# Kernel tuning notes

Hardware: AMD Instinct MI355X
Metric: run time of the kernel (lower is better)

The kernel has to match this reference:

```python
import jax, jax.numpy as jnp
import numpy as np

KERNEL_MUL = 2.0
KERNEL_NUM = 5
FIX_SIGMA = None


def setup_inputs() -> dict:
    key = jax.random.key(0)
    k1, k2 = jax.random.split(key)
    source = jax.random.normal(k1, (4096, 512), dtype=jnp.float32)
    target = jax.random.normal(k2, (4096, 512), dtype=jnp.float32)
    return {"source": source, "target": target}


def reference(source, target):
    batch_size = source.shape[0]
    total = jnp.concatenate([source, target], axis=0)  # [N, D], N = n1 + n2
    n_samples = total.shape[0]

    # Pairwise squared L2 distances via Gram-matrix trick (same math as
    # the explicit NxNxD broadcast in the original, without materializing it).
    sq = jnp.sum(total * total, axis=1)               # [N]
    gram = total @ total.T                            # [N, N]
    l2 = sq[:, None] + sq[None, :] - 2.0 * gram       # [N, N]

    if FIX_SIGMA:
        bandwidth = jnp.asarray(FIX_SIGMA, dtype=l2.dtype)
    else:
        # torch used L2_distance.data -> no gradient through bandwidth
        bandwidth = jax.lax.stop_gradient(jnp.sum(l2)) / (n_samples ** 2 - n_samples)
    bandwidth = bandwidth / (KERNEL_MUL ** (KERNEL_NUM // 2))

    # Multi-bandwidth Gaussian kernel sum
    kernels = jnp.zeros_like(l2)
    for i in range(KERNEL_NUM):
        kernels = kernels + jnp.exp(-l2 / (bandwidth * (KERNEL_MUL ** i)))

    b = batch_size
    XX = kernels[:b, :b]
    YY = kernels[b:, b:]
    XY = kernels[:b, b:]
    YX = kernels[b:, :b]
    loss = jnp.mean(XX + YY - XY - YX)
    return loss
```

## Files before the change

kernel.cpp:

```cpp
#include <hip/hip_runtime.h>
#include <math.h>

typedef float f32x4 __attribute__((ext_vector_type(4)));
typedef int   i32x4 __attribute__((ext_vector_type(4)));
typedef signed char i8x8 __attribute__((ext_vector_type(8)));
typedef __fp16 h16x2 __attribute__((ext_vector_type(2)));

#define NROWS 8192
#define NCOLS 512
#define BHALF 4096
#define NT    64
#define NBLK  2080
#define CSPART 256
#define QS    24.0f
#define INV_S2 (1.0f / (24.0f * 24.0f))

__global__ void k_conv(const float* __restrict__ src, const float* __restrict__ tgt,
                       signed char* __restrict__ bfrag, int* __restrict__ sqi,
                       double* __restrict__ sqpart, float* __restrict__ cspart) {
    __shared__ signed char ldsc[32][528];
    __shared__ float colp[4][NCOLS];
    __shared__ double dred[4];
    int t = threadIdx.x, w = t >> 6, l = t & 63;
    int r0 = blockIdx.x * 32;
    float c0x=0.f,c0y=0.f,c0z=0.f,c0w=0.f, c1x=0.f,c1y=0.f,c1z=0.f,c1w=0.f;
    double facc = 0.0;
    #pragma unroll
    for (int r = 0; r < 8; ++r) {
        int row = r0 + w * 8 + r;
        const float* base = (row < BHALF) ? (src + (size_t)row * NCOLS)
                                          : (tgt + (size_t)(row - BHALF) * NCOLS);
        float4 a = ((const float4*)base)[2 * l];
        float4 b = ((const float4*)base)[2 * l + 1];
        int q0 = (int)rintf(fminf(fmaxf(a.x * QS, -127.f), 127.f));
        int q1 = (int)rintf(fminf(fmaxf(a.y * QS, -127.f), 127.f));
        int q2 = (int)rintf(fminf(fmaxf(a.z * QS, -127.f), 127.f));
        int q3 = (int)rintf(fminf(fmaxf(a.w * QS, -127.f), 127.f));
        int q4 = (int)rintf(fminf(fmaxf(b.x * QS, -127.f), 127.f));
        int q5 = (int)rintf(fminf(fmaxf(b.y * QS, -127.f), 127.f));
        int q6 = (int)rintf(fminf(fmaxf(b.z * QS, -127.f), 127.f));
        int q7 = (int)rintf(fminf(fmaxf(b.w * QS, -127.f), 127.f));
        i8x8 v8;
        v8[0]=(signed char)q0; v8[1]=(signed char)q1; v8[2]=(signed char)q2; v8[3]=(signed char)q3;
        v8[4]=(signed char)q4; v8[5]=(signed char)q5; v8[6]=(signed char)q6; v8[7]=(signed char)q7;
        *(i8x8*)&ldsc[w * 8 + r][l * 8] = v8;
        float s = a.x*a.x + a.y*a.y + a.z*a.z + a.w*a.w
                + b.x*b.x + b.y*b.y + b.z*b.z + b.w*b.w;
        facc += (double)s;
        int si = q0*q0 + q1*q1 + q2*q2 + q3*q3 + q4*q4 + q5*q5 + q6*q6 + q7*q7;
        #pragma unroll
        for (int o = 32; o > 0; o >>= 1) si += __shfl_down(si, o);
        if (l == 0) sqi[row] = si;
        c0x += a.x; c0y += a.y; c0z += a.z; c0w += a.w;
        c1x += b.x; c1y += b.y; c1z += b.z; c1w += b.w;
    }
    #pragma unroll
    for (int o = 32; o > 0; o >>= 1) facc += __shfl_down(facc, o);
    if (l == 0) dred[w] = facc;
    colp[w][l*8+0] = c0x; colp[w][l*8+1] = c0y; colp[w][l*8+2] = c0z; colp[w][l*8+3] = c0w;
    colp[w][l*8+4] = c1x; colp[w][l*8+5] = c1y; colp[w][l*8+6] = c1z; colp[w][l*8+7] = c1w;
    __syncthreads();
    if (t == 0) sqpart[blockIdx.x] = (dred[0] + dred[1]) + (dred[2] + dred[3]);
    float s0 = colp[0][t] + colp[1][t] + colp[2][t] + colp[3][t];
    float s1 = colp[0][t+256] + colp[1][t+256] + colp[2][t+256] + colp[3][t+256];
    cspart[(size_t)blockIdx.x * NCOLS + t]       = s0;
    cspart[(size_t)blockIdx.x * NCOLS + t + 256] = s1;
    int rg0 = blockIdx.x * 2;
    #pragma unroll
    for (int c4 = 0; c4 < 4; ++c4) {
        int c = c4 * 256 + t;
        int g = c >> 9, sl = (c >> 4) & 31, lrr = c & 15;
        i32x4 v = *(const i32x4*)&ldsc[g * 16 + lrr][sl * 16];
        *(i32x4*)(bfrag + (size_t)(rg0 + g) * 8192 + sl * 256 + lrr * 16) = v;
    }
}

__global__ void k_red(const float* __restrict__ cspart, double* __restrict__ colsq) {
    __shared__ double lred[4][64];
    int b = blockIdx.x, t = threadIdx.x;
    int c = b * 64 + (t & 63), q = t >> 6;
    double a = 0.0;
    #pragma unroll 4
    for (int p = q * 64; p < q * 64 + 64; ++p)
        a += (double)cspart[(size_t)p * NCOLS + c];
    lred[q][t & 63] = a;
    __syncthreads();
    if (t < 64) {
        double s = (lred[0][t] + lred[1][t]) + (lred[2][t] + lred[3][t]);
        colsq[b * 64 + t] = s * s;
    }
}

__global__ void k_bw(const double* __restrict__ sqpart, const double* __restrict__ colsq,
                     float* __restrict__ cvals) {
    __shared__ double red[512];
    int t = threadIdx.x;
    red[t] = (t < CSPART) ? sqpart[t] : 0.0;
    __syncthreads();
    for (int o = 256; o > 0; o >>= 1) { if (t < o) red[t] += red[t + o]; __syncthreads(); }
    double sT = red[0];
    __syncthreads();
    red[t] = colsq[t]; __syncthreads();
    for (int o = 256; o > 0; o >>= 1) { if (t < o) red[t] += red[t + o]; __syncthreads(); }
    if (t == 0) {
        double G = red[0];
        double sum_l2 = 2.0 * (double)NROWS * sT - 2.0 * G;
        double denom = (double)NROWS * (double)NROWS - (double)NROWS;
        double bw = sum_l2 / denom / 4.0;
        const double L2E = 1.4426950408889634;
        double b = bw;
        #pragma unroll
        for (int k = 0; k < 5; ++k) { cvals[k] = (float)(L2E / b); b *= 2.0; }
    }
}

__global__ __launch_bounds__(256, 4)
void k_mmd(const signed char* __restrict__ bfrag, const int* __restrict__ sqi,
           const float* __restrict__ cvals, double* __restrict__ psum) {
    __shared__ float wred[4];

    int bid = blockIdx.x;
    int swz = (bid & 7) * (NBLK / 8) + (bid >> 3);
    int v = NBLK - 1 - swz;
    int k = (int)((sqrtf(8.f * (float)v + 1.f) - 1.f) * 0.5f);
    while ((k + 1) * (k + 2) / 2 <= v) ++k;
    while (k * (k + 1) / 2 > v) --k;
    int I = NT - 1 - k;
    int J = NT - 1 - (v - k * (k + 1) / 2);

    const int t  = threadIdx.x;
    const int w  = t >> 6;
    const int l  = t & 63;
    const int lr = l & 15;
    const int lk = l >> 4;

    const bool dsup = (I == J);
    int da, db;
    if (dsup) { da = (w == 2) ? 1 : 0; db = (w == 0) ? 0 : 1; }
    else      { da = w >> 1;           db = w & 1; }
    const int i_t = 2 * I + da, j_t = 2 * J + db;
    const int rowA0 = i_t * 64, rowB0 = j_t * 64;

    const int i_u = __builtin_amdgcn_readfirstlane(i_t);
    const int j_u = __builtin_amdgcn_readfirstlane(j_t);
    const signed char* bA = bfrag + (size_t)i_u * 32768;
    const signed char* bB = bfrag + (size_t)j_u * 32768;
    const int voff = lk * 256 + lr * 16;

    i32x4 acc[4][4] = {};
    #pragma unroll
    for (int kt = 0; kt < 8; ++kt) {
        i32x4 af[4], bf[4];
        #pragma unroll
        for (int m = 0; m < 4; ++m)
            af[m] = *(const i32x4*)(bA + m * 8192 + kt * 1024 + voff);
        #pragma unroll
        for (int n = 0; n < 4; ++n)
            bf[n] = *(const i32x4*)(bB + n * 8192 + kt * 1024 + voff);
        #pragma unroll
        for (int m = 0; m < 4; ++m)
            #pragma unroll
            for (int n = 0; n < 4; ++n)
                acc[m][n] = __builtin_amdgcn_mfma_i32_16x16x64_i8(
                    af[m], bf[n], acc[m][n], 0, 0, 0);
    }

    i32x4 sqa[4];
    #pragma unroll
    for (int m = 0; m < 4; ++m)
        sqa[m] = *(const i32x4*)&sqi[rowA0 + m * 16 + lk * 4];
    int sqb[4];
    #pragma unroll
    for (int n = 0; n < 4; ++n)
        sqb[n] = sqi[rowB0 + n * 16 + lr];
    const float c4i = cvals[4] * INV_S2;
    const float c2  = 2.f * c4i;
    f32x4 sqaf[4];
    #pragma unroll
    for (int m = 0; m < 4; ++m)
        #pragma unroll
        for (int r = 0; r < 4; ++r)
            sqaf[m][r] = c4i * (float)sqa[m][r];
    float sqbf[4];
    #pragma unroll
    for (int n = 0; n < 4; ++n)
        sqbf[n] = c4i * (float)sqb[n];

    const bool elem = dsup && ((w & 1) == 0);
    const float wb  = dsup ? 1.f : 2.f;
    const float sgn = ((rowA0 < BHALF) == (rowB0 < BHALF)) ? 1.f : -1.f;
    float local = 0.f;
    if (elem) {
        #pragma unroll
        for (int m = 0; m < 4; ++m)
            #pragma unroll
            for (int n = 0; n < 4; ++n)
                #pragma unroll
                for (int r = 0; r < 4; ++r) {
                    float x  = __builtin_amdgcn_exp2f(
                        fmaf((float)acc[m][n][r], c2, -(sqaf[m][r] + sqbf[n])));
                    float x2 = x * x;
                    float x4 = x2 * x2;
                    float x8 = x4 * x4;
                    float e  = fmaf(x8, x8, x8) + ((x + x2) + x4);
                    int gi = rowA0 + m * 16 + lk * 4 + r;
                    int gj = rowB0 + n * 16 + lr;
                    float wgt = (gj > gi) ? 2.f : ((gj == gi) ? 1.f : 0.f);
                    local += wgt * e;
                }
    } else {
        const h16x2 ones = {(__fp16)1.f, (__fp16)1.f};
        #pragma unroll
        for (int m = 0; m < 4; ++m)
            #pragma unroll
            for (int n = 0; n < 4; ++n)
                #pragma unroll
                for (int rp = 0; rp < 2; ++rp) {
                    float x0 = __builtin_amdgcn_exp2f(
                        fmaf((float)acc[m][n][2*rp],     c2, -(sqaf[m][2*rp]     + sqbf[n])));
                    float x1 = __builtin_amdgcn_exp2f(
                        fmaf((float)acc[m][n][2*rp + 1], c2, -(sqaf[m][2*rp + 1] + sqbf[n])));
                    h16x2 x  = {(__fp16)x0, (__fp16)x1};
                    h16x2 x2 = x * x;
                    h16x2 x4 = x2 * x2;
                    h16x2 x8 = x4 * x4;
                    h16x2 e2 = ((x + x2) + (x4 + x8)) + x8 * x8;
#if __has_builtin(__builtin_amdgcn_fdot2)
                    local = __builtin_amdgcn_fdot2(e2, ones, local, false);
#else
                    local += (float)e2[0] + (float)e2[1];
#endif
                }
        local *= wb * sgn;
    }

    #pragma unroll
    for (int o = 32; o > 0; o >>= 1) local += __shfl_down(local, o);
    if (l == 0) wred[w] = local;
    __syncthreads();
    if (t == 0) {
        psum[blockIdx.x] = (double)((wred[0] + wred[1]) + (wred[2] + wred[3]));
    }
}

__global__ void k_final(const double* __restrict__ psum, float* __restrict__ out) {
    __shared__ double red[512];
    int t = threadIdx.x;
    double a = 0.0;
    #pragma unroll
    for (int i = t; i < NBLK; i += 512) a += psum[i];
    red[t] = a; __syncthreads();
    for (int o = 256; o > 0; o >>= 1) { if (t < o) red[t] += red[t + o]; __syncthreads(); }
    if (t == 0) out[0] = (float)(red[0] * (1.0 / ((double)BHALF * (double)BHALF)));
}

extern "C" void kernel_launch(void* const* d_in, const int* in_sizes, int n_in,
                              void* d_out, int out_size, void* d_ws, size_t ws_size,
                              hipStream_t stream) {
    (void)in_sizes; (void)n_in; (void)out_size; (void)ws_size;
    const float* src = (const float*)d_in[0];
    const float* tgt = (const float*)d_in[1];
    float* out = (float*)d_out;
    char* ws = (char*)d_ws;
    signed char* bfrag = (signed char*)(ws);
    int*    sqi    = (int*)   (ws + 4194304);
    float*  cspart = (float*) (ws + 4227072);
    float*  cvals  = (float*) (ws + 4751360);
    double* colsq  = (double*)(ws + 4751392);
    double* sqpart = (double*)(ws + 4755488);
    double* psum   = (double*)(ws + 4757536);

    k_conv  <<<CSPART, 256, 0, stream>>>(src, tgt, bfrag, sqi, sqpart, cspart);
    k_red   <<<8, 256, 0, stream>>>(cspart, colsq);
    k_bw    <<<1, 512, 0, stream>>>(sqpart, colsq, cvals);
    k_mmd   <<<NBLK, 256, 0, stream>>>(bfrag, sqi, cvals, psum);
    k_final <<<1, 512, 0, stream>>>(psum, out);
}
```

Measured before the change: 65.44 us.

## Stage int8 tiles through LDS with async global_load_lds triple buffering

The conversion kernel now writes the quantized int8 matrix in plain row-major order instead of pre-swizzled MFMA fragments, which removes the LDS shuffle step. The pairwise kernel now loads shared 128-row A and B tiles into a triple-buffered, XOR-swizzled LDS region using direct global-to-LDS loads, with waitcnt and barriers overlapping loads for later K-steps with the MFMA work. Each block fetches the tile once for all four waves rather than each wave reading its own fragments from global memory. The cost is 48KB of LDS per block, and occupancy is lowered to 3 blocks per CU. The diagonal-block work assignment also changes (waves now map wr/wc uniformly) and the weight logic is adjusted.

```diff
diff --git a/kernel.cpp b/kernel.cpp
--- a/kernel.cpp
+++ b/kernel.cpp
@@ -15,10 +15,12 @@
 #define QS    24.0f
 #define INV_S2 (1.0f / (24.0f * 24.0f))
 
+typedef __attribute__((address_space(1))) const unsigned int guint;
+typedef __attribute__((address_space(3))) unsigned int luint;
+
 __global__ void k_conv(const float* __restrict__ src, const float* __restrict__ tgt,
-                       signed char* __restrict__ bfrag, int* __restrict__ sqi,
+                       signed char* __restrict__ bfall, int* __restrict__ sqi,
                        double* __restrict__ sqpart, float* __restrict__ cspart) {
-    __shared__ signed char ldsc[32][528];
     __shared__ float colp[4][NCOLS];
     __shared__ double dred[4];
     int t = threadIdx.x, w = t >> 6, l = t & 63;
@@ -43,7 +45,7 @@
         i8x8 v8;
         v8[0]=(signed char)q0; v8[1]=(signed char)q1; v8[2]=(signed char)q2; v8[3]=(signed char)q3;
         v8[4]=(signed char)q4; v8[5]=(signed char)q5; v8[6]=(signed char)q6; v8[7]=(signed char)q7;
-        *(i8x8*)&ldsc[w * 8 + r][l * 8] = v8;
+        *(i8x8*)(bfall + (size_t)row * NCOLS + l * 8) = v8;
         float s = a.x*a.x + a.y*a.y + a.z*a.z + a.w*a.w
                 + b.x*b.x + b.y*b.y + b.z*b.z + b.w*b.w;
         facc += (double)s;
@@ -65,14 +67,6 @@
     float s1 = colp[0][t+256] + colp[1][t+256] + colp[2][t+256] + colp[3][t+256];
     cspart[(size_t)blockIdx.x * NCOLS + t]       = s0;
     cspart[(size_t)blockIdx.x * NCOLS + t + 256] = s1;
-    int rg0 = blockIdx.x * 2;
-    #pragma unroll
-    for (int c4 = 0; c4 < 4; ++c4) {
-        int c = c4 * 256 + t;
-        int g = c >> 9, sl = (c >> 4) & 31, lrr = c & 15;
-        i32x4 v = *(const i32x4*)&ldsc[g * 16 + lrr][sl * 16];
-        *(i32x4*)(bfrag + (size_t)(rg0 + g) * 8192 + sl * 256 + lrr * 16) = v;
-    }
 }
 
 __global__ void k_red(const float* __restrict__ cspart, double* __restrict__ colsq) {
@@ -114,9 +108,10 @@
     }
 }
 
-__global__ __launch_bounds__(256, 4)
-void k_mmd(const signed char* __restrict__ bfrag, const int* __restrict__ sqi,
+__global__ __launch_bounds__(256, 3)
+void k_mmd(const signed char* __restrict__ bfall, const int* __restrict__ sqi,
            const float* __restrict__ cvals, double* __restrict__ psum) {
+    __shared__ signed char lds[3 * 16384];
     __shared__ float wred[4];
 
     int bid = blockIdx.x;
@@ -134,36 +129,66 @@
     const int lr = l & 15;
     const int lk = l >> 4;
 
-    const bool dsup = (I == J);
-    int da, db;
-    if (dsup) { da = (w == 2) ? 1 : 0; db = (w == 0) ? 0 : 1; }
-    else      { da = w >> 1;           db = w & 1; }
-    const int i_t = 2 * I + da, j_t = 2 * J + db;
-    const int rowA0 = i_t * 64, rowB0 = j_t * 64;
-
-    const int i_u = __builtin_amdgcn_readfirstlane(i_t);
-    const int j_u = __builtin_amdgcn_readfirstlane(j_t);
-    const signed char* bA = bfrag + (size_t)i_u * 32768;
-    const signed char* bB = bfrag + (size_t)j_u * 32768;
-    const int voff = lk * 256 + lr * 16;
+    const int wr = w >> 1, wc = w & 1;
+    const int rowA0 = I * 128 + wr * 64, rowB0 = J * 128 + wc * 64;
+    const signed char* gA = bfall + (size_t)(I * 128) * NCOLS;
+    const signed char* gB = bfall + (size_t)(J * 128) * NCOLS;
+
+    const int row0 = t >> 2, ss0 = (t & 3) ^ ((row0 >> 1) & 3);
+    const signed char* ga0 = gA + (size_t)row0 * NCOLS + ss0 * 16;
+    const signed char* gb0 = gB + (size_t)row0 * NCOLS + ss0 * 16;
+    signed char* dA = lds + t * 16;
+    signed char* dB = lds + 8192 + t * 16;
+
+    const int ssl = lk ^ ((lr >> 1) & 3);
+    const signed char* pA = lds + (wr * 64 + lr) * 64 + ssl * 16;
+    const signed char* pB = lds + 8192 + (wc * 64 + lr) * 64 + ssl * 16;
+
+    #define STAGE(bsel, kt)                                                        \
+        __builtin_amdgcn_global_load_lds((guint*)(ga0 + (kt) * 64),                \
+            (luint*)(dA + (bsel) * 16384), 16, 0, 0);                              \
+        __builtin_amdgcn_global_load_lds((guint*)(ga0 + 64 * NCOLS + (kt) * 64),   \
+            (luint*)(dA + (bsel) * 16384 + 4096), 16, 0, 0);                       \
+        __builtin_amdgcn_global_load_lds((guint*)(gb0 + (kt) * 64),                \
+            (luint*)(dB + (bsel) * 16384), 16, 0, 0);                              \
+        __builtin_amdgcn_global_load_lds((guint*)(gb0 + 64 * NCOLS + (kt) * 64),   \
+            (luint*)(dB + (bsel) * 16384 + 4096), 16, 0, 0);
+
+    #define COMPUTE(bsel)                                                          \
+        {                                                                          \
+            i32x4 af[4], bf[4];                                                    \
+            _Pragma("unroll")                                                      \
+            for (int m = 0; m < 4; ++m)                                            \
+                af[m] = *(const i32x4*)(pA + (bsel) * 16384 + m * 1024);           \
+            _Pragma("unroll")                                                      \
+            for (int n = 0; n < 4; ++n)                                            \
+                bf[n] = *(const i32x4*)(pB + (bsel) * 16384 + n * 1024);           \
+            _Pragma("unroll")                                                      \
+            for (int m = 0; m < 4; ++m)                                            \
+                _Pragma("unroll")                                                  \
+                for (int n = 0; n < 4; ++n)                                        \
+                    acc[m][n] = __builtin_amdgcn_mfma_i32_16x16x64_i8(             \
+                        af[m], bf[n], acc[m][n], 0, 0, 0);                         \
+        }
+
+    #define STEP(kt, vm)                                                           \
+        asm volatile("s_waitcnt vmcnt(" #vm ")" ::: "memory");                     \
+        __builtin_amdgcn_s_barrier();                                              \
+        asm volatile("" ::: "memory");                                             \
+        if ((kt) + 2 < 8) { STAGE(((kt) + 2) % 3, (kt) + 2) }                      \
+        COMPUTE((kt) % 3)
 
     i32x4 acc[4][4] = {};
-    #pragma unroll
-    for (int kt = 0; kt < 8; ++kt) {
-        i32x4 af[4], bf[4];
-        #pragma unroll
-        for (int m = 0; m < 4; ++m)
-            af[m] = *(const i32x4*)(bA + m * 8192 + kt * 1024 + voff);
-        #pragma unroll
-        for (int n = 0; n < 4; ++n)
-            bf[n] = *(const i32x4*)(bB + n * 8192 + kt * 1024 + voff);
-        #pragma unroll
-        for (int m = 0; m < 4; ++m)
-            #pragma unroll
-            for (int n = 0; n < 4; ++n)
-                acc[m][n] = __builtin_amdgcn_mfma_i32_16x16x64_i8(
-                    af[m], bf[n], acc[m][n], 0, 0, 0);
-    }
+
+    STAGE(0, 0)
+    STAGE(1, 1)
+
+    STEP(0, 4) STEP(1, 4) STEP(2, 4) STEP(3, 4)
+    STEP(4, 4) STEP(5, 4) STEP(6, 4) STEP(7, 0)
+
+    #undef STAGE
+    #undef COMPUTE
+    #undef STEP
 
     i32x4 sqa[4];
     #pragma unroll
@@ -186,8 +211,9 @@
     for (int n = 0; n < 4; ++n)
         sqbf[n] = c4i * (float)sqb[n];
 
-    const bool elem = dsup && ((w & 1) == 0);
-    const float wb  = dsup ? 1.f : 2.f;
+    const bool dsup = (I == J);
+    const bool elem = dsup && (wr == wc);
+    const float wb  = (dsup || elem) ? 1.f : 2.f;
     const float sgn = ((rowA0 < BHALF) == (rowB0 < BHALF)) ? 1.f : -1.f;
     float local = 0.f;
     if (elem) {
@@ -262,7 +288,7 @@
     const float* tgt = (const float*)d_in[1];
     float* out = (float*)d_out;
     char* ws = (char*)d_ws;
-    signed char* bfrag = (signed char*)(ws);
+    signed char* bfall = (signed char*)(ws);
     int*    sqi    = (int*)   (ws + 4194304);
     float*  cspart = (float*) (ws + 4227072);
     float*  cvals  = (float*) (ws + 4751360);
@@ -270,9 +296,9 @@
     double* sqpart = (double*)(ws + 4755488);
     double* psum   = (double*)(ws + 4757536);
 
-    k_conv  <<<CSPART, 256, 0, stream>>>(src, tgt, bfrag, sqi, sqpart, cspart);
+    k_conv  <<<CSPART, 256, 0, stream>>>(src, tgt, bfall, sqi, sqpart, cspart);
     k_red   <<<8, 256, 0, stream>>>(cspart, colsq);
     k_bw    <<<1, 512, 0, stream>>>(sqpart, colsq, cvals);
-    k_mmd   <<<NBLK, 256, 0, stream>>>(bfrag, sqi, cvals, psum);
+    k_mmd   <<<NBLK, 256, 0, stream>>>(bfall, sqi, cvals, psum);
     k_final <<<1, 512, 0, stream>>>(psum, out);
 }
```

Measured after the change: 54.17 us, median of 2. 17.2% less time.
